# Kernel optimization log

Measured on AMD Instinct MI355X. Metric: run time of the kernel, lower is better.

Reference implementation:

```python
import jax, jax.numpy as jnp
import numpy as np


def _gcn_conv(x, edge_index, W, b):
    """PyG GCNConv: add self-loops, symmetric normalization, scatter-add aggregation."""
    N = x.shape[0]
    loops = jnp.arange(N, dtype=edge_index.dtype)
    src = jnp.concatenate([edge_index[0], loops])  # [E+N]
    dst = jnp.concatenate([edge_index[1], loops])  # [E+N]
    # degree computed on destination nodes (flow: source_to_target)
    deg = jax.ops.segment_sum(jnp.ones_like(dst, dtype=x.dtype), dst, num_segments=N)
    deg_inv_sqrt = jnp.where(deg > 0, jax.lax.rsqrt(jnp.maximum(deg, 1.0)), 0.0)
    norm = deg_inv_sqrt[src] * deg_inv_sqrt[dst]  # [E+N]
    h = x @ W  # [N, out]
    msg = h[src] * norm[:, None]  # [E+N, out]
    out = jax.ops.segment_sum(msg, dst, num_segments=N)
    return out + b


def setup_inputs() -> dict:
    key = jax.random.key(0)
    k1, k2, k3, k4 = jax.random.split(key, 4)
    N, E, D_IN, D_HID, D_OUT = 100000, 1600000, 128, 128, 64
    x = jax.random.normal(k1, (N, D_IN), dtype=jnp.float32)
    edge_index = jax.random.randint(k2, (2, E), 0, N, dtype=jnp.int64)
    batch = jnp.zeros((N,), dtype=jnp.int64)
    W1 = jax.random.normal(k3, (D_IN, D_HID), dtype=jnp.float32) / np.sqrt(D_IN)
    b1 = jnp.zeros((D_HID,), dtype=jnp.float32)
    W2 = jax.random.normal(k4, (D_HID, D_OUT), dtype=jnp.float32) / np.sqrt(D_HID)
    b2 = jnp.zeros((D_OUT,), dtype=jnp.float32)
    return {"x": x, "edge_index": edge_index, "batch": batch,
            "W1": W1, "b1": b1, "W2": W2, "b2": b2}


def reference(x, edge_index, batch, W1, b1, W2, b2):
    h = _gcn_conv(x, edge_index, W1, b1)
    h = jax.nn.relu(h)
    # dropout is identity at inference (training=False)
    out = _gcn_conv(h, edge_index, W2, b2)
    # original computes F.log_softmax but discards it; returns out
    return out
```

## Files before the change

kernel.cpp:

```cpp
#include <hip/hip_runtime.h>
#include <hip/hip_fp16.h>


#define KDIM 128
#define BSHIFT 9
#define BSIZE 512
#define ECHUNK 8192
#define PACK_SHIFT 20
#define PACK_MASK ((1u << PACK_SHIFT) - 1)

typedef _Float16 h8 __attribute__((ext_vector_type(8)));
typedef float f4v __attribute__((ext_vector_type(4)));


__global__ void bcount_kernel(const int* __restrict__ dst, int* __restrict__ bhist,
                              int E, int NB) {
    __shared__ int lcnt[256];
    const int t = threadIdx.x;
    lcnt[t] = 0;
    __syncthreads();
    const int base = blockIdx.x * ECHUNK;
#pragma unroll
    for (int j = 0; j < ECHUNK / 256; j++) {
        int e = base + j * 256 + t;
        if (e < E) atomicAdd(&lcnt[dst[e] >> BSHIFT], 1);
    }
    __syncthreads();
    if (t < NB && lcnt[t]) atomicAdd(&bhist[t], lcnt[t]);
}

__global__ void bscan_kernel(const int* __restrict__ bhist, int* __restrict__ bbase,
                             int* __restrict__ bcursor, int NB, int E) {
    __shared__ int tmp[256];
    const int t = threadIdx.x;
    tmp[t] = (t < NB) ? bhist[t] : 0;
    __syncthreads();
    for (int off = 1; off < 256; off <<= 1) {
        int x = (t >= off) ? tmp[t - off] : 0;
        __syncthreads();
        if (t >= off) tmp[t] += x;
        __syncthreads();
    }
    int exc = (t == 0) ? 0 : tmp[t - 1];
    if (t < NB) {
        bbase[t] = exc;
        bcursor[t] = exc;
    }
    if (t == 0) bbase[NB] = E;
}


__launch_bounds__(256) __global__
void bscatter_kernel(const int* __restrict__ src, const int* __restrict__ dst,
                     int* __restrict__ bcursor, unsigned int* __restrict__ packed_out,
                     int E, int NB) {
    __shared__ int lcnt[256];
    __shared__ int lexc[256];
    __shared__ int lbase[256];
    __shared__ unsigned int lpacked[ECHUNK];
    __shared__ unsigned char lbslot[ECHUNK];

    const int t = threadIdx.x;
    lcnt[t] = 0;
    __syncthreads();

    const int base = blockIdx.x * ECHUNK;
    const int cnt = min(ECHUNK, E - base);

#pragma unroll
    for (int j = 0; j < ECHUNK / 256; j++) {
        int e = base + j * 256 + t;
        if (e < E) atomicAdd(&lcnt[dst[e] >> BSHIFT], 1);
    }
    __syncthreads();

    lexc[t] = lcnt[t];
    __syncthreads();
    for (int off = 1; off < 256; off <<= 1) {
        int x = (t >= off) ? lexc[t - off] : 0;
        __syncthreads();
        if (t >= off) lexc[t] += x;
        __syncthreads();
    }
    int inc = lexc[t];
    __syncthreads();
    lexc[t] = inc - lcnt[t];

    if (t < NB && lcnt[t]) lbase[t] = atomicAdd(&bcursor[t], lcnt[t]);

    lcnt[t] = lexc[t];
    __syncthreads();

#pragma unroll
    for (int j = 0; j < ECHUNK / 256; j++) {
        int e = base + j * 256 + t;
        if (e < E) {
            int d = dst[e];
            int b = d >> BSHIFT;
            int pos = atomicAdd(&lcnt[b], 1);
            lpacked[pos] = (unsigned int)src[e] | ((unsigned int)(d & (BSIZE - 1)) << PACK_SHIFT);
            lbslot[pos] = (unsigned char)b;
        }
    }
    __syncthreads();

#pragma unroll
    for (int j = 0; j < ECHUNK / 256; j++) {
        int s = j * 256 + t;
        if (s < cnt) {
            int b = lbslot[s];
            packed_out[lbase[b] + (s - lexc[b])] = lpacked[s];
        }
    }
}


__launch_bounds__(256) __global__
void bplace_kernel(const unsigned int* __restrict__ packed, const int* __restrict__ bbase,
                   int* __restrict__ rowptr, float* __restrict__ dinv,
                   int* __restrict__ ssrc, int N, int E) {
    __shared__ int ncnt[BSIZE];
    __shared__ int nexc[BSIZE];
    __shared__ int s1[256];

    const int t = threadIdx.x;
    const int b = blockIdx.x;
    ncnt[t] = 0;
    ncnt[t + 256] = 0;
    __syncthreads();

    const int e0 = bbase[b];
    const int e1 = bbase[b + 1];
    for (int e = e0 + t; e < e1; e += 256) {
        atomicAdd(&ncnt[packed[e] >> PACK_SHIFT], 1);
    }
    __syncthreads();

    const int a0 = ncnt[2 * t];
    const int a1 = ncnt[2 * t + 1];
    s1[t] = a0 + a1;
    __syncthreads();
    for (int off = 1; off < 256; off <<= 1) {
        int x = (t >= off) ? s1[t - off] : 0;
        __syncthreads();
        if (t >= off) s1[t] += x;
        __syncthreads();
    }
    const int base2 = (t == 0) ? 0 : s1[t - 1];
    nexc[2 * t] = base2;
    nexc[2 * t + 1] = base2 + a0;

    const int nodebase = b * BSIZE;
    const int n0 = nodebase + 2 * t;
    const int n1 = n0 + 1;
    if (n0 < N) {
        rowptr[n0] = e0 + base2;
        dinv[n0] = rsqrtf((float)(a0 + 1));
    }
    if (n1 < N) {
        rowptr[n1] = e0 + base2 + a0;
        dinv[n1] = rsqrtf((float)(a1 + 1));
    }
    if (b == 0 && t == 0) rowptr[N] = E;
    __syncthreads();

    for (int e = e0 + t; e < e1; e += 256) {
        unsigned int p = packed[e];
        int d = p >> PACK_SHIFT;
        int pos = e0 + atomicAdd(&nexc[d], 1);
        ssrc[pos] = (int)(p & PACK_MASK);
    }
}


__device__ inline h8 pack8(float4 u, float4 v) {
    h8 r;
    r[0] = (_Float16)u.x; r[1] = (_Float16)u.y; r[2] = (_Float16)u.z; r[3] = (_Float16)u.w;
    r[4] = (_Float16)v.x; r[5] = (_Float16)v.y; r[6] = (_Float16)v.z; r[7] = (_Float16)v.w;
    return r;
}

template <int DOUT, bool AHALF>
__launch_bounds__(256) __global__
void gemm_mfma_kernel(const void* __restrict__ Xv, const float* __restrict__ W,
                      const float* __restrict__ dinv, _Float16* __restrict__ outh, int N) {
    constexpr int K = KDIM;
    constexpr int KS = K + 8;
    constexpr int NT = DOUT / 16;
    __shared__ _Float16 Wl[DOUT * KS];

    const int t = threadIdx.x;
    const int wave = t >> 6;
    const int lane = t & 63;
    const int l15 = lane & 15;
    const int quad = lane >> 4;

#pragma unroll
    for (int i = t; i < DOUT * (K / 4); i += 256) {
        int n = i & (DOUT - 1);
        int kg = i / DOUT;
        union { _Float16 h[4]; uint2 u; } tmp;
#pragma unroll
        for (int j = 0; j < 4; j++)
            tmp.h[j] = (_Float16)W[(size_t)(kg * 4 + j) * DOUT + n];
        *(uint2*)(&Wl[n * KS + kg * 4]) = tmp.u;
    }
    __syncthreads();

    const int rowbase = blockIdx.x * 128;
    const int row0 = rowbase + wave * 32 + l15;
    const int row1 = row0 + 16;
    const int rc0 = min(row0, N - 1);
    const int rc1 = min(row1, N - 1);

    f4v acc[2][NT];
#pragma unroll
    for (int r = 0; r < 2; r++)
#pragma unroll
        for (int ct = 0; ct < NT; ct++) acc[r][ct] = (f4v)0.0f;

#pragma unroll
    for (int kc = 0; kc < K; kc += 32) {
        const int kof = kc + quad * 8;
        h8 a0, a1;
        if (AHALF) {
            const _Float16* Xh = (const _Float16*)Xv;
            a0 = *(const h8*)(Xh + (size_t)rc0 * K + kof);
            a1 = *(const h8*)(Xh + (size_t)rc1 * K + kof);
        } else {
            const float* Xf = (const float*)Xv;
            const float* p0 = Xf + (size_t)rc0 * K + kof;
            const float* p1 = Xf + (size_t)rc1 * K + kof;
            a0 = pack8(*(const float4*)p0, *(const float4*)(p0 + 4));
            a1 = pack8(*(const float4*)p1, *(const float4*)(p1 + 4));
        }
#pragma unroll
        for (int ct = 0; ct < NT; ct++) {
            h8 b = *(const h8*)(&Wl[(size_t)(ct * 16 + l15) * KS + kof]);
            acc[0][ct] = __builtin_amdgcn_mfma_f32_16x16x32_f16(a0, b, acc[0][ct], 0, 0, 0);
            acc[1][ct] = __builtin_amdgcn_mfma_f32_16x16x32_f16(a1, b, acc[1][ct], 0, 0, 0);
        }
    }

#pragma unroll
    for (int r = 0; r < 2; r++) {
        const int rb = rowbase + wave * 32 + r * 16 + quad * 4;
#pragma unroll
        for (int g = 0; g < 4; g++) {
            int row = rb + g;
            if (row < N) {
                float di = dinv[row];
                _Float16* op = outh + (size_t)row * DOUT + l15;
#pragma unroll
                for (int ct = 0; ct < NT; ct++)
                    op[ct * 16] = (_Float16)(acc[r][ct][g] * di);
            }
        }
    }
}


template <int DOUT, bool RELU, bool HOUT>
__launch_bounds__(256) __global__
void agg_kernel(const __half* __restrict__ hs, const int* __restrict__ rowptr,
                const int* __restrict__ ssrc, const float* __restrict__ dinv,
                const float* __restrict__ bias, void* __restrict__ outv, int N) {
    constexpr int TPN = DOUT / 8;
    const int npb = blockDim.x / TPN;
    const int node = blockIdx.x * npb + threadIdx.x / TPN;
    if (node >= N) return;
    const int lane = threadIdx.x % TPN;
    const int c0 = lane * 8;

    float acc[8];
    {
        uint4 u = *(const uint4*)(hs + (size_t)node * DOUT + c0);
        const __half2* hp = (const __half2*)&u;
#pragma unroll
        for (int q = 0; q < 4; q++) {
            float2 f = __half22float2(hp[q]);
            acc[2 * q] = f.x;
            acc[2 * q + 1] = f.y;
        }
    }

    const int e0 = rowptr[node];
    const int e1 = rowptr[node + 1];
    int e = e0;
    for (; e + 4 <= e1; e += 4) {
        int s0 = ssrc[e + 0];
        int s1 = ssrc[e + 1];
        int s2 = ssrc[e + 2];
        int s3 = ssrc[e + 3];
        uint4 u0 = *(const uint4*)(hs + (size_t)s0 * DOUT + c0);
        uint4 u1 = *(const uint4*)(hs + (size_t)s1 * DOUT + c0);
        uint4 u2 = *(const uint4*)(hs + (size_t)s2 * DOUT + c0);
        uint4 u3 = *(const uint4*)(hs + (size_t)s3 * DOUT + c0);
        const __half2* p0 = (const __half2*)&u0;
        const __half2* p1 = (const __half2*)&u1;
        const __half2* p2 = (const __half2*)&u2;
        const __half2* p3 = (const __half2*)&u3;
#pragma unroll
        for (int q = 0; q < 4; q++) {
            float2 f0 = __half22float2(p0[q]);
            float2 f1 = __half22float2(p1[q]);
            float2 f2 = __half22float2(p2[q]);
            float2 f3 = __half22float2(p3[q]);
            acc[2 * q]     += (f0.x + f1.x) + (f2.x + f3.x);
            acc[2 * q + 1] += (f0.y + f1.y) + (f2.y + f3.y);
        }
    }
    for (; e < e1; e++) {
        int s = ssrc[e];
        uint4 u = *(const uint4*)(hs + (size_t)s * DOUT + c0);
        const __half2* hp = (const __half2*)&u;
#pragma unroll
        for (int q = 0; q < 4; q++) {
            float2 f = __half22float2(hp[q]);
            acc[2 * q] += f.x;
            acc[2 * q + 1] += f.y;
        }
    }

    const float di = dinv[node];
    float o[8];
#pragma unroll
    for (int q = 0; q < 2; q++) {
        float4 bq = *(const float4*)(bias + c0 + 4 * q);
        o[4 * q + 0] = di * acc[4 * q + 0] + bq.x;
        o[4 * q + 1] = di * acc[4 * q + 1] + bq.y;
        o[4 * q + 2] = di * acc[4 * q + 2] + bq.z;
        o[4 * q + 3] = di * acc[4 * q + 3] + bq.w;
    }
    if (RELU) {
#pragma unroll
        for (int j = 0; j < 8; j++) o[j] = fmaxf(o[j], 0.f);
    }
    if (HOUT) {
        union { __half2 h[4]; uint4 u; } pk;
#pragma unroll
        for (int q = 0; q < 4; q++)
            pk.h[q] = __floats2half2_rn(o[2 * q], o[2 * q + 1]);
        *(uint4*)((__half*)outv + (size_t)node * DOUT + c0) = pk.u;
    } else {
        float* op = (float*)outv + (size_t)node * DOUT + c0;
        *(float4*)op = make_float4(o[0], o[1], o[2], o[3]);
        *(float4*)(op + 4) = make_float4(o[4], o[5], o[6], o[7]);
    }
}


extern "C" void kernel_launch(void* const* d_in, const int* in_sizes, int n_in,
                              void* d_out, int out_size, void* d_ws, size_t ws_size,
                              hipStream_t stream) {
    const float* x  = (const float*)d_in[0];
    const int*   ei = (const int*)d_in[1];
    const float* W1 = (const float*)d_in[3];
    const float* b1 = (const float*)d_in[4];
    const float* W2 = (const float*)d_in[5];
    const float* b2 = (const float*)d_in[6];
    float* out = (float*)d_out;

    const int N = in_sizes[0] / KDIM;
    const int E = in_sizes[1] / 2;
    const int* esrc = ei;
    const int* edst = ei + E;
    const int NB = (N + BSIZE - 1) >> BSHIFT;

    char* ws = (char*)d_ws;
    size_t off = 0;
    auto alloc = [&](size_t bytes) {
        size_t p = off;
        off = (off + bytes + 511) & ~(size_t)511;
        return p;
    };
    int*      bhist   = (int*)(ws + alloc((size_t)NB * 4));
    int*      bbase   = (int*)(ws + alloc((size_t)(NB + 1) * 4));
    int*      bcursor = (int*)(ws + alloc((size_t)NB * 4));
    int*      rowptr  = (int*)(ws + alloc((size_t)(N + 1) * 4));
    float*    dinv    = (float*)(ws + alloc((size_t)N * 4));
    int*      ssrc    = (int*)(ws + alloc((size_t)E * 4));
    _Float16* hs      = (_Float16*)(ws + alloc((size_t)N * KDIM * 2));
    _Float16* out1    = (_Float16*)(ws + alloc((size_t)N * KDIM * 2));
    unsigned int* packed = (unsigned int*)hs;
    (void)ws_size; (void)n_in; (void)out_size;

    const int eb = (E + ECHUNK - 1) / ECHUNK;

    hipMemsetAsync(bhist, 0, (size_t)NB * 4, stream);

    bcount_kernel<<<eb, 256, 0, stream>>>(edst, bhist, E, NB);
    bscan_kernel<<<1, 256, 0, stream>>>(bhist, bbase, bcursor, NB, E);
    bscatter_kernel<<<eb, 256, 0, stream>>>(esrc, edst, bcursor, packed, E, NB);
    bplace_kernel<<<NB, 256, 0, stream>>>(packed, bbase, rowptr, dinv, ssrc, N, E);

    gemm_mfma_kernel<128, false><<<(N + 127) / 128, 256, 0, stream>>>(x, W1, dinv, hs, N);
    agg_kernel<128, true, true><<<(N + 15) / 16, 256, 0, stream>>>(
        (const __half*)hs, rowptr, ssrc, dinv, b1, out1, N);

    gemm_mfma_kernel<64, true><<<(N + 127) / 128, 256, 0, stream>>>(out1, W2, dinv, hs, N);
    agg_kernel<64, false, false><<<(N + 31) / 32, 256, 0, stream>>>(
        (const __half*)hs, rowptr, ssrc, dinv, b2, out, N);
}
```

Measured before the change: 286.8 us.

## Build CSR via global per-node histogram and multi-block scan before bucket scatter

Replaces the per-bucket histogram and single-block scan with a per-node global-atomic histogram, a two-level exclusive scan over all nodes, and a finalize pass that writes rowptr, dinv and the bucket cursors. The placement kernel then drops its shared-memory count and scan phase and only does atomic slot placement, using 1024 threads per block. ECHUNK is halved so the scatter kernel runs more, smaller blocks. The intent is to remove the serialized per-bucket counting and scan from the critical placement kernel, at the cost of 1.6M global atomics, more launches and an extra memset.

```diff
diff --git a/kernel.cpp b/kernel.cpp
--- a/kernel.cpp
+++ b/kernel.cpp
@@ -5,7 +5,7 @@
 #define KDIM 128
 #define BSHIFT 9
 #define BSIZE 512
-#define ECHUNK 8192
+#define ECHUNK 4096
 #define PACK_SHIFT 20
 #define PACK_MASK ((1u << PACK_SHIFT) - 1)
 
@@ -13,40 +13,71 @@
 typedef float f4v __attribute__((ext_vector_type(4)));
 
 
-__global__ void bcount_kernel(const int* __restrict__ dst, int* __restrict__ bhist,
-                              int E, int NB) {
-    __shared__ int lcnt[256];
-    const int t = threadIdx.x;
-    lcnt[t] = 0;
-    __syncthreads();
-    const int base = blockIdx.x * ECHUNK;
-#pragma unroll
-    for (int j = 0; j < ECHUNK / 256; j++) {
-        int e = base + j * 256 + t;
-        if (e < E) atomicAdd(&lcnt[dst[e] >> BSHIFT], 1);
-    }
-    __syncthreads();
-    if (t < NB && lcnt[t]) atomicAdd(&bhist[t], lcnt[t]);
-}
-
-__global__ void bscan_kernel(const int* __restrict__ bhist, int* __restrict__ bbase,
-                             int* __restrict__ bcursor, int NB, int E) {
+__global__ void hist_kernel(const int* __restrict__ dst, int* __restrict__ hist, int E) {
+    int i = blockIdx.x * blockDim.x + threadIdx.x;
+    if (i < E) atomicAdd(&hist[dst[i]], 1);
+}
+
+__global__ void scan1_kernel(const int* __restrict__ hist, int* __restrict__ exc,
+                             int* __restrict__ bsums, int n) {
     __shared__ int tmp[256];
-    const int t = threadIdx.x;
-    tmp[t] = (t < NB) ? bhist[t] : 0;
+    int t = threadIdx.x;
+    int base = blockIdx.x * 1024 + t * 4;
+    int v[4];
+    int s = 0;
+#pragma unroll
+    for (int j = 0; j < 4; j++) {
+        int idx = base + j;
+        int h = (idx < n) ? hist[idx] : 0;
+        v[j] = s;
+        s += h;
+    }
+    tmp[t] = s;
     __syncthreads();
     for (int off = 1; off < 256; off <<= 1) {
-        int x = (t >= off) ? tmp[t - off] : 0;
+        int x = 0;
+        if (t >= off) x = tmp[t - off];
         __syncthreads();
         if (t >= off) tmp[t] += x;
         __syncthreads();
     }
-    int exc = (t == 0) ? 0 : tmp[t - 1];
-    if (t < NB) {
-        bbase[t] = exc;
-        bcursor[t] = exc;
-    }
-    if (t == 0) bbase[NB] = E;
+    int texc = (t == 0) ? 0 : tmp[t - 1];
+    if (t == 255) bsums[blockIdx.x] = tmp[255];
+#pragma unroll
+    for (int j = 0; j < 4; j++) {
+        int idx = base + j;
+        if (idx < n) exc[idx] = texc + v[j];
+    }
+}
+
+__global__ void scan2_kernel(int* __restrict__ bsums, int nb) {
+    __shared__ int tmp[256];
+    int t = threadIdx.x;
+    int val = (t < nb) ? bsums[t] : 0;
+    tmp[t] = val;
+    __syncthreads();
+    for (int off = 1; off < 256; off <<= 1) {
+        int x = 0;
+        if (t >= off) x = tmp[t - off];
+        __syncthreads();
+        if (t >= off) tmp[t] += x;
+        __syncthreads();
+    }
+    int excv = (t == 0) ? 0 : tmp[t - 1];
+    if (t < nb) bsums[t] = excv;
+}
+
+__global__ void finalize_kernel(const int* __restrict__ hist, const int* __restrict__ boff,
+                                int* __restrict__ rowptr, int* __restrict__ bcursor,
+                                float* __restrict__ dinv, int N, int E) {
+    int i = blockIdx.x * blockDim.x + threadIdx.x;
+    if (i < N) {
+        int v = rowptr[i] + boff[i >> 10];
+        rowptr[i] = v;
+        if ((i & (BSIZE - 1)) == 0) bcursor[i >> BSHIFT] = v;
+        dinv[i] = rsqrtf((float)(hist[i] + 1));
+    }
+    if (i == 0) rowptr[N] = E;
 }
 
 
@@ -115,59 +146,24 @@
 }
 
 
-__launch_bounds__(256) __global__
-void bplace_kernel(const unsigned int* __restrict__ packed, const int* __restrict__ bbase,
-                   int* __restrict__ rowptr, float* __restrict__ dinv,
-                   int* __restrict__ ssrc, int N, int E) {
-    __shared__ int ncnt[BSIZE];
-    __shared__ int nexc[BSIZE];
-    __shared__ int s1[256];
-
+__launch_bounds__(1024) __global__
+void place2_kernel(const unsigned int* __restrict__ packed, const int* __restrict__ rowptr,
+                   int* __restrict__ ssrc, int N, int E, int NB) {
+    __shared__ int cur[BSIZE];
     const int t = threadIdx.x;
     const int b = blockIdx.x;
-    ncnt[t] = 0;
-    ncnt[t + 256] = 0;
-    __syncthreads();
-
-    const int e0 = bbase[b];
-    const int e1 = bbase[b + 1];
-    for (int e = e0 + t; e < e1; e += 256) {
-        atomicAdd(&ncnt[packed[e] >> PACK_SHIFT], 1);
-    }
-    __syncthreads();
-
-    const int a0 = ncnt[2 * t];
-    const int a1 = ncnt[2 * t + 1];
-    s1[t] = a0 + a1;
-    __syncthreads();
-    for (int off = 1; off < 256; off <<= 1) {
-        int x = (t >= off) ? s1[t - off] : 0;
-        __syncthreads();
-        if (t >= off) s1[t] += x;
-        __syncthreads();
-    }
-    const int base2 = (t == 0) ? 0 : s1[t - 1];
-    nexc[2 * t] = base2;
-    nexc[2 * t + 1] = base2 + a0;
-
-    const int nodebase = b * BSIZE;
-    const int n0 = nodebase + 2 * t;
-    const int n1 = n0 + 1;
-    if (n0 < N) {
-        rowptr[n0] = e0 + base2;
-        dinv[n0] = rsqrtf((float)(a0 + 1));
-    }
-    if (n1 < N) {
-        rowptr[n1] = e0 + base2 + a0;
-        dinv[n1] = rsqrtf((float)(a1 + 1));
-    }
-    if (b == 0 && t == 0) rowptr[N] = E;
-    __syncthreads();
-
-    for (int e = e0 + t; e < e1; e += 256) {
+    const int nodebase = b << BSHIFT;
+    const int nn = min(BSIZE, N - nodebase);
+
+    if (t < nn) cur[t] = rowptr[nodebase + t];
+    __syncthreads();
+
+    const int e0 = rowptr[nodebase];
+    const int e1 = (b == NB - 1) ? E : rowptr[nodebase + BSIZE];
+    for (int e = e0 + t; e < e1; e += 1024) {
         unsigned int p = packed[e];
         int d = p >> PACK_SHIFT;
-        int pos = e0 + atomicAdd(&nexc[d], 1);
+        int pos = atomicAdd(&cur[d], 1);
         ssrc[pos] = (int)(p & PACK_MASK);
     }
 }
@@ -374,10 +370,10 @@
         off = (off + bytes + 511) & ~(size_t)511;
         return p;
     };
-    int*      bhist   = (int*)(ws + alloc((size_t)NB * 4));
-    int*      bbase   = (int*)(ws + alloc((size_t)(NB + 1) * 4));
+    int*      hist    = (int*)(ws + alloc((size_t)N * 4));
+    int*      rowptr  = (int*)(ws + alloc((size_t)(N + 1) * 4));
     int*      bcursor = (int*)(ws + alloc((size_t)NB * 4));
-    int*      rowptr  = (int*)(ws + alloc((size_t)(N + 1) * 4));
+    int*      bsums   = (int*)(ws + alloc(256 * 4));
     float*    dinv    = (float*)(ws + alloc((size_t)N * 4));
     int*      ssrc    = (int*)(ws + alloc((size_t)E * 4));
     _Float16* hs      = (_Float16*)(ws + alloc((size_t)N * KDIM * 2));
@@ -386,13 +382,16 @@
     (void)ws_size; (void)n_in; (void)out_size;
 
     const int eb = (E + ECHUNK - 1) / ECHUNK;
-
-    hipMemsetAsync(bhist, 0, (size_t)NB * 4, stream);
-
-    bcount_kernel<<<eb, 256, 0, stream>>>(edst, bhist, E, NB);
-    bscan_kernel<<<1, 256, 0, stream>>>(bhist, bbase, bcursor, NB, E);
+    const int nb = (N + 1023) / 1024;
+
+    hipMemsetAsync(hist, 0, (size_t)N * 4, stream);
+
+    hist_kernel<<<(E + 255) / 256, 256, 0, stream>>>(edst, hist, E);
+    scan1_kernel<<<nb, 256, 0, stream>>>(hist, rowptr, bsums, N);
+    scan2_kernel<<<1, 256, 0, stream>>>(bsums, nb);
+    finalize_kernel<<<(N + 255) / 256, 256, 0, stream>>>(hist, bsums, rowptr, bcursor, dinv, N, E);
     bscatter_kernel<<<eb, 256, 0, stream>>>(esrc, edst, bcursor, packed, E, NB);
-    bplace_kernel<<<NB, 256, 0, stream>>>(packed, bbase, rowptr, dinv, ssrc, N, E);
+    place2_kernel<<<NB, 1024, 0, stream>>>(packed, rowptr, ssrc, N, E, NB);
 
     gemm_mfma_kernel<128, false><<<(N + 127) / 128, 256, 0, stream>>>(x, W1, dinv, hs, N);
     agg_kernel<128, true, true><<<(N + 15) / 16, 256, 0, stream>>>(
```

After: 325.4 us. +13.4%, slower.
